# Kernel optimization log

Measured on AMD Instinct MI355X. Metric: run time of the kernel, lower is better.

## Reference

```python
import jax, jax.numpy as jnp
import numpy as np

N = 100000      # nodes
E = 1600000     # edges
F_IN = 512      # num_feat
HID = 128       # hidden dim (hardcoded in GNN)
ENC = 64        # encoder_dim
NCLS = 10       # num_classes
DOM = 40        # domain head hidden (hardcoded)


def setup_inputs() -> dict:
    key = jax.random.key(0)
    ks = jax.random.split(key, 16)
    def lin(k, fi, fo):
        kw, kb = jax.random.split(k)
        s = 1.0 / np.sqrt(fi)
        return (jax.random.uniform(kw, (fi, fo), jnp.float32, -s, s),
                jax.random.uniform(kb, (fo,), jnp.float32, -s, s))
    W1, b1 = lin(ks[0], F_IN, HID)
    W2, b2 = lin(ks[1], HID, ENC)
    att_w, att_b = lin(ks[2], ENC, 1)
    cls_w, cls_b = lin(ks[3], ENC, NCLS)
    dw1, db1 = lin(ks[4], ENC, DOM)
    dw2, db2 = lin(ks[5], DOM, 2)
    return {
        "x": jax.random.normal(ks[6], (N, F_IN), jnp.float32),
        "edge_index": jax.random.randint(ks[7], (2, E), 0, N, jnp.int64),
        "ppmi_edge_weight": jax.random.uniform(ks[8], (E,), jnp.float32, 0.01, 1.0),
        "rate": 1,
        "W1": W1, "b1": b1, "W2": W2, "b2": b2,
        "att_w": att_w, "att_b": att_b,
        "cls_w": cls_w, "cls_b": cls_b,
        "dw1": dw1, "db1": db1, "dw2": dw2, "db2": db2,
    }


def _edge_norm(src, dst, w):
    # symmetric normalization d^-1/2 * w * d^-1/2 (self-loops already included)
    deg = jax.ops.segment_sum(w, dst, num_segments=N)
    dinv = jnp.where(deg > 0, jax.lax.rsqrt(deg), 0.0)
    return dinv[src] * w * dinv[dst]


def _conv(h, W, b, src, dst, enorm):
    h = h @ W                                   # [N, out]
    msg = h[src] * enorm[:, None]               # [E+N, out] gather
    return jax.ops.segment_sum(msg, dst, num_segments=N) + b


def _encode(x, src, dst, enorm, W1, b1, W2, b2):
    h = jax.nn.relu(_conv(x, W1, b1, src, dst, enorm))  # dropout = identity (eval)
    return _conv(h, W2, b2, src, dst, enorm)


def reference(x, edge_index, ppmi_edge_weight, rate,
              W1, b1, W2, b2, att_w, att_b,
              cls_w, cls_b, dw1, db1, dw2, db2):
    loop = jnp.arange(N, dtype=edge_index.dtype)
    src = jnp.concatenate([edge_index[0], loop])
    dst = jnp.concatenate([edge_index[1], loop])
    ones_w = jnp.ones(src.shape[0], jnp.float32)
    ppmi_w = jnp.concatenate([ppmi_edge_weight, jnp.ones(N, jnp.float32)])

    gcn_norm = _edge_norm(src, dst, ones_w)
    ppmi_norm = _edge_norm(src, dst, ppmi_w)

    # both encoders share weights (base_model=self.encoder)
    g = _encode(x, src, dst, gcn_norm, W1, b1, W2, b2)    # [N, ENC]
    p = _encode(x, src, dst, ppmi_norm, W1, b1, W2, b2)   # [N, ENC]

    stacked = jnp.stack([g, p], axis=1)                   # [N, 2, ENC]
    logits = stacked @ att_w + att_b                      # [N, 2, 1]
    wts = jax.nn.softmax(logits, axis=1)
    emb = jnp.sum(stacked * wts, axis=1)                  # [N, ENC]

    class_predict = emb @ cls_w + cls_b
    r = jnp.float32(rate)
    # gradient reversal: identity fwd, -rate * grad bwd
    rev = jax.lax.stop_gradient((1.0 + r) * emb) - r * emb
    h = jax.nn.relu(rev @ dw1 + db1)                      # dropout = identity (eval)
    domain_predict = h @ dw2 + db2
    return emb, class_predict, domain_predict
```

## Files before the change

kernel.cpp:

```cpp
#include <hip/hip_runtime.h>
#include <math.h>
#include <stdint.h>

#define NND  100000
#define NED  1600000
#define FIN  512
#define HID  128
#define ENC  64
#define NCLS 10
#define DOM  40

#define SCAN_BS 256
#define NBS ((NND + SCAN_BS - 1) / SCAN_BS)

typedef __attribute__((ext_vector_type(8))) short short8v;
typedef __attribute__((ext_vector_type(8))) unsigned short ushort8v;
typedef __attribute__((ext_vector_type(4))) float f32x4;
typedef __attribute__((ext_vector_type(4))) unsigned int uint4v;


__global__ void k_deg_rank(const int* __restrict__ dst, const float* __restrict__ ppmi,
                           unsigned long long* __restrict__ packed,
                           int* __restrict__ rank) {
  int e = blockIdx.x * blockDim.x + threadIdx.x;
  if (e >= NED) return;
  int d = dst[e];
  unsigned int fx = (unsigned int)(ppmi[e] * 1073741824.0f + 0.5f);
  unsigned long long v = (1ull << 40) | (unsigned long long)fx;
  unsigned long long old = atomicAdd(&packed[d], v);
  rank[e] = (int)(old >> 40);
}

__global__ void k_dinv(const unsigned long long* __restrict__ packed,
                       float* __restrict__ dinv_g, float* __restrict__ dinv_p) {
  int i = blockIdx.x * blockDim.x + threadIdx.x;
  if (i >= NND) return;
  unsigned long long pk = packed[i];
  float cnt = (float)(unsigned int)(pk >> 40);
  float dp  = (float)(pk & 0xFFFFFFFFFFull) * (1.0f / 1073741824.0f);
  dinv_g[i] = 1.0f / sqrtf(cnt + 1.0f);
  dinv_p[i] = 1.0f / sqrtf(dp + 1.0f);
}


__global__ void k_scan_a(const unsigned long long* __restrict__ packed,
                         int* __restrict__ psum) {
  __shared__ int s[SCAN_BS];
  int t = threadIdx.x, i = blockIdx.x * SCAN_BS + t;
  s[t] = (i < NND) ? (int)(packed[i] >> 40) : 0;
  __syncthreads();
  for (int o = SCAN_BS / 2; o; o >>= 1) {
    if (t < o) s[t] += s[t + o];
    __syncthreads();
  }
  if (t == 0) psum[blockIdx.x] = s[0];
}

__global__ void k_scan_b(int* __restrict__ psum) {
  __shared__ int s[512];
  int t = threadIdx.x;
  int v = (t < NBS) ? psum[t] : 0;
  s[t] = v;
  __syncthreads();
  for (int o = 1; o < 512; o <<= 1) {
    int add = (t >= o) ? s[t - o] : 0;
    __syncthreads();
    s[t] += add;
    __syncthreads();
  }
  if (t < NBS) psum[t] = s[t] - v;
}

__global__ void k_scan_c(const unsigned long long* __restrict__ packed,
                         const int* __restrict__ psum, int* __restrict__ row_ptr) {
  __shared__ int s[SCAN_BS];
  int t = threadIdx.x, i = blockIdx.x * SCAN_BS + t;
  int v = (i < NND) ? (int)(packed[i] >> 40) : 0;
  s[t] = v;
  __syncthreads();
  for (int o = 1; o < SCAN_BS; o <<= 1) {
    int add = (t >= o) ? s[t - o] : 0;
    __syncthreads();
    s[t] += add;
    __syncthreads();
  }
  if (i < NND) row_ptr[i] = psum[blockIdx.x] + s[t] - v;
  if (i == NND - 1) row_ptr[NND] = psum[blockIdx.x] + s[t];
}


__global__ void k_scatter(const int* __restrict__ src, const int* __restrict__ dst,
                          const float* __restrict__ ppmi,
                          const int* __restrict__ row_ptr, const int* __restrict__ rank,
                          const float* __restrict__ dinv_g, const float* __restrict__ dinv_p,
                          int4* __restrict__ csr) {
  int e = blockIdx.x * blockDim.x + threadIdx.x;
  if (e >= NED) return;
  int s = src[e], d = dst[e];
  int pos = row_ptr[d] + rank[e];
  int4 rec;
  rec.x = s;
  rec.y = __float_as_int(dinv_g[s] * dinv_g[d]);
  rec.z = __float_as_int(dinv_p[s] * ppmi[e] * dinv_p[d]);
  rec.w = 0;
  csr[pos] = rec;
}


template<int NC>
__global__ void k_bprep(const float* __restrict__ B, ushort* __restrict__ bhi,
                        ushort* __restrict__ blo, int K) {
  int id = blockIdx.x * 256 + threadIdx.x;
  if (id >= K * NC) return;
  int k = id / NC, c = id % NC;
  float x = B[id];
  unsigned int u = __float_as_uint(x);
  ushort h = (ushort)(u >> 16);
  float lo = x - __uint_as_float(u & 0xffff0000u);
  ushort l = (ushort)(__float_as_uint(lo) >> 16);
  size_t o = ((size_t)(k >> 3) * NC + c) * 8 + (k & 7);
  bhi[o] = h;
  blo[o] = l;
}


__device__ inline void split8(const float4 a, const float4 b,
                              short8v& hi, short8v& lo) {
  float f[8] = {a.x, a.y, a.z, a.w, b.x, b.y, b.z, b.w};
  uint4v H, L;
#pragma unroll
  for (int i = 0; i < 4; ++i) {
    unsigned int u0 = __float_as_uint(f[2 * i]);
    unsigned int u1 = __float_as_uint(f[2 * i + 1]);
    H[i] = (u0 >> 16) | (u1 & 0xffff0000u);
    float l0 = f[2 * i]     - __uint_as_float(u0 & 0xffff0000u);
    float l1 = f[2 * i + 1] - __uint_as_float(u1 & 0xffff0000u);
    L[i] = (__float_as_uint(l0) >> 16) | (__float_as_uint(l1) & 0xffff0000u);
  }
  hi = __builtin_bit_cast(short8v, H);
  lo = __builtin_bit_cast(short8v, L);
}

__device__ inline ushort f2bf_rne(float x) {
  unsigned int u = __float_as_uint(x);
  unsigned int r = u + 0x7fffu + ((u >> 16) & 1u);
  return (ushort)(r >> 16);
}

__device__ inline float bf2f(unsigned short v) {
  return __uint_as_float((unsigned int)v << 16);
}


__device__ inline void gload_lds16(const float* gp, float* lp) {
  __builtin_amdgcn_global_load_lds(
      (const __attribute__((address_space(1))) void*)gp,
      (__attribute__((address_space(3))) void*)lp, 16, 0, 0);
}

__global__ __launch_bounds__(256, 3) void gemm1_lds(
    const float* __restrict__ A, const ushort* __restrict__ Bhi,
    const ushort* __restrict__ Blo, ushort* __restrict__ C) {
  __shared__ float At[2][128 * 32];
  const int tid = threadIdx.x;
  const int lane = tid & 63;
  const int w = tid >> 6;
  const int wr = w >> 1, wc = w & 1;
  const int g = lane >> 4;
  const int l16 = lane & 15;
  const int row_base = blockIdx.x * 128;

  size_t srow[4]; int scol[4];
  {
    int e = w * 256 + lane * 4;
#pragma unroll
    for (int i = 0; i < 4; ++i) {
      int ee = e + i * 1024;
      int r = ee >> 5;
      int chunk_lds = (ee >> 2) & 7;
      int chunk_g = chunk_lds ^ (r & 7);
      int rr = row_base + r; if (rr >= NND) rr = NND - 1;
      srow[i] = (size_t)rr * FIN;
      scol[i] = chunk_g * 4;
    }
  }

  int coln[4];
#pragma unroll
  for (int n = 0; n < 4; ++n) coln[n] = wc * 64 + n * 16 + l16;
  int arow_l[4];
#pragma unroll
  for (int m = 0; m < 4; ++m) arow_l[m] = wr * 64 + m * 16 + l16;

  f32x4 acc[4][4] = {};

#pragma unroll
  for (int i = 0; i < 4; ++i)
    gload_lds16(A + srow[i] + 0 + scol[i], &At[0][w * 256 + i * 1024]);
  __syncthreads();

  for (int t = 0; t < FIN / 32; ++t) {
    const int cur = t & 1;
    if (t + 1 < FIN / 32) {
      const int k0n = (t + 1) * 32;
#pragma unroll
      for (int i = 0; i < 4; ++i)
        gload_lds16(A + srow[i] + k0n + scol[i], &At[cur ^ 1][w * 256 + i * 1024]);
    }

    short8v ah[4], al[4];
#pragma unroll
    for (int m = 0; m < 4; ++m) {
      int r = arow_l[m];
      int c0 = (((g * 2)     ^ (r & 7)) << 2);
      int c1 = (((g * 2 + 1) ^ (r & 7)) << 2);
      float4 a0 = *(const float4*)&At[cur][r * 32 + c0];
      float4 a1 = *(const float4*)&At[cur][r * 32 + c1];
      split8(a0, a1, ah[m], al[m]);
    }

    short8v bh[4], bl[4];
    const int kc = t * 4 + g;
#pragma unroll
    for (int n = 0; n < 4; ++n) {
      size_t off = ((size_t)kc * HID + coln[n]) * 8;
      bh[n] = *(const short8v*)(Bhi + off);
      bl[n] = *(const short8v*)(Blo + off);
    }

#pragma unroll
    for (int m = 0; m < 4; ++m)
#pragma unroll
      for (int n = 0; n < 4; ++n) {
        acc[m][n] = __builtin_amdgcn_mfma_f32_16x16x32_bf16(ah[m], bh[n], acc[m][n], 0, 0, 0);
        acc[m][n] = __builtin_amdgcn_mfma_f32_16x16x32_bf16(al[m], bh[n], acc[m][n], 0, 0, 0);
        acc[m][n] = __builtin_amdgcn_mfma_f32_16x16x32_bf16(ah[m], bl[n], acc[m][n], 0, 0, 0);
      }

    __syncthreads();
  }

#pragma unroll
  for (int m = 0; m < 4; ++m)
#pragma unroll
    for (int i = 0; i < 4; ++i) {
      int r = row_base + wr * 64 + m * 16 + g * 4 + i;
      if (r < NND) {
#pragma unroll
        for (int n = 0; n < 4; ++n)
          C[(size_t)r * HID + coln[n]] = f2bf_rne(acc[m][n][i]);
      }
    }
}


template<int WR>
__global__ __launch_bounds__(256, 4) void gemm2_split(
    const ushort* __restrict__ As, const ushort* __restrict__ Bhi,
    const ushort* __restrict__ Blo, ushort* __restrict__ C,
    int M, int K, int Nc) {
  const int lane = threadIdx.x & 63;
  const int w = threadIdx.x >> 6;
  const int g = lane >> 4;
  const int l16 = lane & 15;
  const int row_base = blockIdx.x * (WR * 64) + w * 64;

  size_t arow[4];
#pragma unroll
  for (int m = 0; m < 4; ++m) {
    int r = row_base + m * 16 + l16;
    if (r >= M) r = M - 1;
    arow[m] = (size_t)r * K;
  }
  int coln[4];
#pragma unroll
  for (int n = 0; n < 4; ++n) coln[n] = n * 16 + l16;

  f32x4 acc[4][4] = {};

  for (int k0 = 0; k0 < K; k0 += 32) {
    short8v ah[4];
#pragma unroll
    for (int m = 0; m < 4; ++m)
      ah[m] = *(const short8v*)(As + arow[m] + k0 + g * 8);
    short8v bh[4], bl[4];
    const int kc = (k0 >> 3) + g;
#pragma unroll
    for (int n = 0; n < 4; ++n) {
      size_t off = ((size_t)kc * Nc + coln[n]) * 8;
      bh[n] = *(const short8v*)(Bhi + off);
      bl[n] = *(const short8v*)(Blo + off);
    }
#pragma unroll
    for (int m = 0; m < 4; ++m)
#pragma unroll
      for (int n = 0; n < 4; ++n) {
        acc[m][n] = __builtin_amdgcn_mfma_f32_16x16x32_bf16(ah[m], bh[n], acc[m][n], 0, 0, 0);
        acc[m][n] = __builtin_amdgcn_mfma_f32_16x16x32_bf16(ah[m], bl[n], acc[m][n], 0, 0, 0);
      }
  }

#pragma unroll
  for (int m = 0; m < 4; ++m)
#pragma unroll
    for (int i = 0; i < 4; ++i) {
      int r = row_base + m * 16 + g * 4 + i;
      if (r < M) {
#pragma unroll
        for (int n = 0; n < 4; ++n) {
          int c = coln[n];
          size_t o = (r < NND) ? ((size_t)r * 128 + c)
                               : ((size_t)(r - NND) * 128 + 64 + c);
          C[o] = f2bf_rne(acc[m][n][i]);
        }
      }
    }
}


__global__ __launch_bounds__(256) void k_agg1(
    const ushort* __restrict__ hlinb, const int* __restrict__ row_ptr,
    const int4* __restrict__ csr,
    const float* __restrict__ dinv_g, const float* __restrict__ dinv_p,
    const float* __restrict__ b1, ushort* __restrict__ hhs) {
  int wid = (blockIdx.x * blockDim.x + threadIdx.x) >> 6;
  int lane = threadIdx.x & 63;
  if (wid >= NND) return;
  const int gp = lane >> 4;
  const int t  = lane & 15;
  float sg = dinv_g[wid]; sg *= sg;
  float sp = dinv_p[wid]; sp *= sp;

  float ag[8] = {}, ap[8] = {};
  if (gp == 0) {
    ushort8v v = *(const ushort8v*)(hlinb + (size_t)wid * HID + 8 * t);
#pragma unroll
    for (int i = 0; i < 8; ++i) {
      float f = bf2f(v[i]);
      ag[i] = f * sg; ap[i] = f * sp;
    }
  }
  int e0 = row_ptr[wid], e1 = row_ptr[wid + 1];
  int k = e0 + gp;
  if (k < e1) {
    int4 rec = csr[k];
    while (true) {
      int kn = k + 4;
      int4 nrec = csr[kn < e1 ? kn : k];
      float wg = __int_as_float(rec.y);
      float wp = __int_as_float(rec.z);
      ushort8v u = *(const ushort8v*)(hlinb + (size_t)rec.x * HID + 8 * t);
#pragma unroll
      for (int i = 0; i < 8; ++i) {
        float f = bf2f(u[i]);
        ag[i] = fmaf(f, wg, ag[i]);
        ap[i] = fmaf(f, wp, ap[i]);
      }
      if (kn >= e1) break;
      k = kn; rec = nrec;
    }
  }
#pragma unroll
  for (int i = 0; i < 8; ++i) {
    ag[i] += __shfl_xor(ag[i], 32); ap[i] += __shfl_xor(ap[i], 32);
    ag[i] += __shfl_xor(ag[i], 16); ap[i] += __shfl_xor(ap[i], 16);
  }

  float bb[8];
  *(float4*)&bb[0] = *(const float4*)(b1 + 8 * t);
  *(float4*)&bb[4] = *(const float4*)(b1 + 8 * t + 4);
  if (gp == 0 || gp == 2) {
    ushort8v outv;
#pragma unroll
    for (int i = 0; i < 8; ++i) {
      float v = (gp == 0) ? fmaxf(ag[i] + bb[i], 0.f) : fmaxf(ap[i] + bb[i], 0.f);
      outv[i] = f2bf_rne(v);
    }
    size_t row = (gp == 0) ? (size_t)wid : (size_t)(NND + wid);
    *(ushort8v*)(hhs + row * HID + 8 * t) = outv;
  }
}


__global__ __launch_bounds__(256) void k_agg2(
    const ushort* __restrict__ h2b, const int* __restrict__ row_ptr,
    const int4* __restrict__ csr,
    const float* __restrict__ dinv_g, const float* __restrict__ dinv_p,
    const float* __restrict__ b2, const float* __restrict__ att_w,
    const float* __restrict__ att_b, float* __restrict__ out_emb) {
  int wid = (blockIdx.x * blockDim.x + threadIdx.x) >> 6;
  int lane = threadIdx.x & 63;
  if (wid >= NND) return;
  const int gp = lane >> 4;
  const int t  = lane & 15;
  const int br = t >> 3;
  const int f0 = (t & 7) * 8;
  float sg = dinv_g[wid]; sg *= sg;
  float sp = dinv_p[wid]; sp *= sp;
  const float sw = br ? sp : sg;

  float acc[8] = {};
  if (gp == 0) {
    ushort8v v = *(const ushort8v*)(h2b + (size_t)wid * 128 + 8 * t);
#pragma unroll
    for (int i = 0; i < 8; ++i) acc[i] = bf2f(v[i]) * sw;
  }
  int e0 = row_ptr[wid], e1 = row_ptr[wid + 1];
  int k = e0 + gp;
  if (k < e1) {
    int4 rec = csr[k];
    while (true) {
      int kn = k + 4;
      int4 nrec = csr[kn < e1 ? kn : k];
      float w = __int_as_float(br ? rec.z : rec.y);
      ushort8v u = *(const ushort8v*)(h2b + (size_t)rec.x * 128 + 8 * t);
#pragma unroll
      for (int i = 0; i < 8; ++i) acc[i] = fmaf(bf2f(u[i]), w, acc[i]);
      if (kn >= e1) break;
      k = kn; rec = nrec;
    }
  }
#pragma unroll
  for (int i = 0; i < 8; ++i) {
    acc[i] += __shfl_xor(acc[i], 32);
    acc[i] += __shfl_xor(acc[i], 16);
  }

  float bb[8];
  *(float4*)&bb[0] = *(const float4*)(b2 + f0);
  *(float4*)&bb[4] = *(const float4*)(b2 + f0 + 4);
  float v[8];
#pragma unroll
  for (int i = 0; i < 8; ++i) v[i] = acc[i] + bb[i];

  float aw[8];
  *(float4*)&aw[0] = *(const float4*)(att_w + f0);
  *(float4*)&aw[4] = *(const float4*)(att_w + f0 + 4);
  float part = 0.f;
#pragma unroll
  for (int i = 0; i < 8; ++i) part = fmaf(v[i], aw[i], part);
  part += __shfl_xor(part, 4);
  part += __shfl_xor(part, 2);
  part += __shfl_xor(part, 1);
  float other = __shfl_xor(part, 8);
  float ab = att_b[0];
  float lg = (br ? other : part) + ab;
  float lp = (br ? part : other) + ab;
  float mx = fmaxf(lg, lp);
  float eg = expf(lg - mx), ep2 = expf(lp - mx);
  float wsm = eg / (eg + ep2);

  float ov[8];
#pragma unroll
  for (int i = 0; i < 8; ++i) ov[i] = __shfl_xor(v[i], 8);
  if (gp == 0 && br == 0) {
    float4* dst = (float4*)(out_emb + (size_t)wid * 64 + f0);
    float4 o0, o1;
    o0.x = wsm * v[0] + (1.f - wsm) * ov[0];
    o0.y = wsm * v[1] + (1.f - wsm) * ov[1];
    o0.z = wsm * v[2] + (1.f - wsm) * ov[2];
    o0.w = wsm * v[3] + (1.f - wsm) * ov[3];
    o1.x = wsm * v[4] + (1.f - wsm) * ov[4];
    o1.y = wsm * v[5] + (1.f - wsm) * ov[5];
    o1.z = wsm * v[6] + (1.f - wsm) * ov[6];
    o1.w = wsm * v[7] + (1.f - wsm) * ov[7];
    dst[0] = o0;
    dst[1] = o1;
  }
}


__global__ __launch_bounds__(128) void k_head(
    const float* __restrict__ emb,
    const float* __restrict__ cls_w, const float* __restrict__ cls_b,
    const float* __restrict__ dw1, const float* __restrict__ db1,
    const float* __restrict__ dw2, const float* __restrict__ db2,
    float* __restrict__ out_cls, float* __restrict__ out_dom) {
  __shared__ float se[128 * 65];
  const int t = threadIdx.x;
  const int base = blockIdx.x * 128;
  for (int c = 0; c < 64; ++c) {
    int idx = c * 128 + t;
    int nl = idx >> 6, k = idx & 63;
    size_t g = (size_t)base * ENC + idx;
    float v = (g < (size_t)NND * ENC) ? emb[g] : 0.f;
    se[nl * 65 + k] = v;
  }
  __syncthreads();

  int node = base + t;
  float c[NCLS], hd[DOM];
#pragma unroll
  for (int j = 0; j < NCLS; ++j) c[j] = cls_b[j];
#pragma unroll
  for (int j = 0; j < DOM; ++j) hd[j] = db1[j];

  for (int k = 0; k < ENC; ++k) {
    float ev = se[t * 65 + k];
#pragma unroll
    for (int j = 0; j < NCLS; ++j) c[j] += ev * cls_w[k * NCLS + j];
#pragma unroll
    for (int j = 0; j < DOM; ++j) hd[j] += ev * dw1[k * DOM + j];
  }
  float d0 = db2[0], d1 = db2[1];
#pragma unroll
  for (int j = 0; j < DOM; ++j) {
    float hv = fmaxf(hd[j], 0.f);
    d0 += hv * dw2[j * 2];
    d1 += hv * dw2[j * 2 + 1];
  }
  if (node < NND) {
#pragma unroll
    for (int j = 0; j < NCLS; ++j) out_cls[(size_t)node * NCLS + j] = c[j];
    out_dom[(size_t)node * 2]     = d0;
    out_dom[(size_t)node * 2 + 1] = d1;
  }
}


extern "C" void kernel_launch(void* const* d_in, const int* in_sizes, int n_in,
                              void* d_out, int out_size, void* d_ws, size_t ws_size,
                              hipStream_t stream) {
  const float* x     = (const float*)d_in[0];
  const int*   ei    = (const int*)d_in[1];
  const float* ppmi  = (const float*)d_in[2];
  const float* W1    = (const float*)d_in[4];
  const float* b1    = (const float*)d_in[5];
  const float* W2    = (const float*)d_in[6];
  const float* b2    = (const float*)d_in[7];
  const float* att_w = (const float*)d_in[8];
  const float* att_b = (const float*)d_in[9];
  const float* cls_w = (const float*)d_in[10];
  const float* cls_b = (const float*)d_in[11];
  const float* dw1   = (const float*)d_in[12];
  const float* db1   = (const float*)d_in[13];
  const float* dw2   = (const float*)d_in[14];
  const float* db2   = (const float*)d_in[15];

  const int* src = ei;
  const int* dst = ei + NED;

  uintptr_t p = (uintptr_t)d_ws;
  auto alloc = [&](size_t bytes) -> void* {
    void* r = (void*)p;
    p += (bytes + 255) & ~(size_t)255;
    return r;
  };
  unsigned long long* packed = (unsigned long long*)alloc((size_t)NND * 8);
  int*    rank    = (int*)   alloc((size_t)NED * 4);
  int*    row_ptr = (int*)   alloc((size_t)(NND + 1) * 4);
  int*    psum    = (int*)   alloc((size_t)NBS * 4);
  float*  dinv_g  = (float*) alloc((size_t)NND * 4);
  float*  dinv_p  = (float*) alloc((size_t)NND * 4);
  int4*   csr     = (int4*)  alloc((size_t)NED * 16);
  ushort* b1hi    = (ushort*)alloc((size_t)FIN * HID * 2);
  ushort* b1lo    = (ushort*)alloc((size_t)FIN * HID * 2);
  ushort* b2hi    = (ushort*)alloc((size_t)HID * ENC * 2);
  ushort* b2lo    = (ushort*)alloc((size_t)HID * ENC * 2);
  ushort* h2b     = (ushort*)alloc((size_t)NND * HID * 2);
  ushort* hhs     = (ushort*)alloc((size_t)2 * NND * HID * 2);

  float* out_emb = (float*)d_out;
  float* out_cls = (float*)d_out + (size_t)NND * ENC;
  float* out_dom = (float*)d_out + (size_t)NND * (ENC + NCLS);

  ushort* h_linb = (ushort*)d_out;

  hipMemsetAsync(packed, 0, (size_t)NND * 8, stream);

  k_deg_rank<<<NED / 256, 256, 0, stream>>>(dst, ppmi, packed, rank);
  k_dinv<<<(NND + 255) / 256, 256, 0, stream>>>(packed, dinv_g, dinv_p);
  k_scan_a<<<NBS, SCAN_BS, 0, stream>>>(packed, psum);
  k_scan_b<<<1, 512, 0, stream>>>(psum);
  k_scan_c<<<NBS, SCAN_BS, 0, stream>>>(packed, psum, row_ptr);
  k_scatter<<<NED / 256, 256, 0, stream>>>(src, dst, ppmi, row_ptr, rank,
                                           dinv_g, dinv_p, csr);

  k_bprep<HID><<<(FIN * HID + 255) / 256, 256, 0, stream>>>(W1, b1hi, b1lo, FIN);
  k_bprep<ENC><<<(HID * ENC + 255) / 256, 256, 0, stream>>>(W2, b2hi, b2lo, HID);

  gemm1_lds<<<(NND + 127) / 128, 256, 0, stream>>>(x, b1hi, b1lo, h_linb);
  k_agg1<<<(NND * 64) / 256, 256, 0, stream>>>(h_linb, row_ptr, csr,
                                               dinv_g, dinv_p, b1, hhs);
  gemm2_split<4><<<(2 * NND + 255) / 256, 256, 0, stream>>>(
      hhs, b2hi, b2lo, h2b, 2 * NND, HID, ENC);
  k_agg2<<<(NND * 64) / 256, 256, 0, stream>>>(h2b, row_ptr, csr,
                                               dinv_g, dinv_p, b2, att_w, att_b, out_emb);

  k_head<<<(NND + 127) / 128, 128, 0, stream>>>(out_emb, cls_w, cls_b, dw1, db1,
                                                dw2, db2, out_cls, out_dom);
}
```

Before: 455.9 us.

## Co-schedule degree counting with GEMM1, shrink CSR records to packed bf16 weights

Merges the edge degree/rank atomic pass into the first GEMM launch by giving every eighth block the atomic work, so the memory-latency-bound atomics overlap with the MFMA-heavy GEMM. It also fuses the two weight-prep launches into one and the dinv computation into the first scan kernel, which cuts launch count. CSR records drop from 16 to 8 bytes by storing both edge norms as bf16 in one word, halving the index/weight traffic in both aggregation passes. The cost is extra rounding of the normalisation weights to bf16 and some GEMM blocks sharing the CUs with atomic-heavy blocks.

```diff
diff --git a/kernel.cpp b/kernel.cpp
--- a/kernel.cpp
+++ b/kernel.cpp
@@ -13,41 +13,200 @@
 #define SCAN_BS 256
 #define NBS ((NND + SCAN_BS - 1) / SCAN_BS)
 
+#define NDEG   96
+#define NGEMM  782
+#define NPH1   (NGEMM + NDEG)
+
 typedef __attribute__((ext_vector_type(8))) short short8v;
 typedef __attribute__((ext_vector_type(8))) unsigned short ushort8v;
 typedef __attribute__((ext_vector_type(4))) float f32x4;
 typedef __attribute__((ext_vector_type(4))) unsigned int uint4v;
 
 
-__global__ void k_deg_rank(const int* __restrict__ dst, const float* __restrict__ ppmi,
-                           unsigned long long* __restrict__ packed,
-                           int* __restrict__ rank) {
-  int e = blockIdx.x * blockDim.x + threadIdx.x;
-  if (e >= NED) return;
-  int d = dst[e];
-  unsigned int fx = (unsigned int)(ppmi[e] * 1073741824.0f + 0.5f);
-  unsigned long long v = (1ull << 40) | (unsigned long long)fx;
-  unsigned long long old = atomicAdd(&packed[d], v);
-  rank[e] = (int)(old >> 40);
-}
-
-__global__ void k_dinv(const unsigned long long* __restrict__ packed,
-                       float* __restrict__ dinv_g, float* __restrict__ dinv_p) {
-  int i = blockIdx.x * blockDim.x + threadIdx.x;
-  if (i >= NND) return;
-  unsigned long long pk = packed[i];
-  float cnt = (float)(unsigned int)(pk >> 40);
-  float dp  = (float)(pk & 0xFFFFFFFFFFull) * (1.0f / 1073741824.0f);
-  dinv_g[i] = 1.0f / sqrtf(cnt + 1.0f);
-  dinv_p[i] = 1.0f / sqrtf(dp + 1.0f);
-}
-
-
-__global__ void k_scan_a(const unsigned long long* __restrict__ packed,
-                         int* __restrict__ psum) {
+__device__ inline void split8(const float4 a, const float4 b,
+                              short8v& hi, short8v& lo) {
+  float f[8] = {a.x, a.y, a.z, a.w, b.x, b.y, b.z, b.w};
+  uint4v H, L;
+#pragma unroll
+  for (int i = 0; i < 4; ++i) {
+    unsigned int u0 = __float_as_uint(f[2 * i]);
+    unsigned int u1 = __float_as_uint(f[2 * i + 1]);
+    H[i] = (u0 >> 16) | (u1 & 0xffff0000u);
+    float l0 = f[2 * i]     - __uint_as_float(u0 & 0xffff0000u);
+    float l1 = f[2 * i + 1] - __uint_as_float(u1 & 0xffff0000u);
+    L[i] = (__float_as_uint(l0) >> 16) | (__float_as_uint(l1) & 0xffff0000u);
+  }
+  hi = __builtin_bit_cast(short8v, H);
+  lo = __builtin_bit_cast(short8v, L);
+}
+
+__device__ inline ushort f2bf_rne(float x) {
+  unsigned int u = __float_as_uint(x);
+  unsigned int r = u + 0x7fffu + ((u >> 16) & 1u);
+  return (ushort)(r >> 16);
+}
+
+__device__ inline float bf2f(unsigned short v) {
+  return __uint_as_float((unsigned int)v << 16);
+}
+
+__device__ inline void gload_lds16(const float* gp, float* lp) {
+  __builtin_amdgcn_global_load_lds(
+      (const __attribute__((address_space(1))) void*)gp,
+      (__attribute__((address_space(3))) void*)lp, 16, 0, 0);
+}
+
+
+__global__ void k_bprep2(const float* __restrict__ W1, ushort* __restrict__ b1hi,
+                         ushort* __restrict__ b1lo, const float* __restrict__ W2,
+                         ushort* __restrict__ b2hi, ushort* __restrict__ b2lo) {
+  int id = blockIdx.x * 256 + threadIdx.x;
+  const float* B; ushort *bhi, *blo; int NC;
+  if (id < FIN * HID) { B = W1; bhi = b1hi; blo = b1lo; NC = HID; }
+  else {
+    id -= FIN * HID;
+    if (id >= HID * ENC) return;
+    B = W2; bhi = b2hi; blo = b2lo; NC = ENC;
+  }
+  int k = id / NC, c = id % NC;
+  float x = B[id];
+  unsigned int u = __float_as_uint(x);
+  ushort h = (ushort)(u >> 16);
+  float lo = x - __uint_as_float(u & 0xffff0000u);
+  ushort l = (ushort)(__float_as_uint(lo) >> 16);
+  size_t o = ((size_t)(k >> 3) * NC + c) * 8 + (k & 7);
+  bhi[o] = h;
+  blo[o] = l;
+}
+
+
+__global__ __launch_bounds__(256, 3) void k_phase1(
+    const float* __restrict__ A, const ushort* __restrict__ Bhi,
+    const ushort* __restrict__ Blo, ushort* __restrict__ C,
+    const int* __restrict__ dst, const float* __restrict__ ppmi,
+    unsigned long long* __restrict__ packed, int* __restrict__ rank) {
+  __shared__ float At[2][128 * 32];
+  const int bi = blockIdx.x;
+
+  if ((bi & 7) == 7 && bi < 768) {
+    int dbi = bi >> 3;
+    for (int e = dbi * 256 + threadIdx.x; e < NED; e += NDEG * 256) {
+      int d = dst[e];
+      unsigned int fx = (unsigned int)(ppmi[e] * 1073741824.0f + 0.5f);
+      unsigned long long v = (1ull << 40) | (unsigned long long)fx;
+      unsigned long long old = atomicAdd(&packed[d], v);
+      rank[e] = (int)(old >> 40);
+    }
+    return;
+  }
+
+  const int gb = (bi < 768) ? (bi - (bi >> 3)) : (bi - NDEG);
+  const int tid = threadIdx.x;
+  const int lane = tid & 63;
+  const int w = tid >> 6;
+  const int wr = w >> 1, wc = w & 1;
+  const int g = lane >> 4;
+  const int l16 = lane & 15;
+  const int row_base = gb * 128;
+
+  size_t srow[4]; int scol[4];
+  {
+    int e = w * 256 + lane * 4;
+#pragma unroll
+    for (int i = 0; i < 4; ++i) {
+      int ee = e + i * 1024;
+      int r = ee >> 5;
+      int chunk_lds = (ee >> 2) & 7;
+      int chunk_g = chunk_lds ^ (r & 7);
+      int rr = row_base + r; if (rr >= NND) rr = NND - 1;
+      srow[i] = (size_t)rr * FIN;
+      scol[i] = chunk_g * 4;
+    }
+  }
+
+  int coln[4];
+#pragma unroll
+  for (int n = 0; n < 4; ++n) coln[n] = wc * 64 + n * 16 + l16;
+  int arow_l[4];
+#pragma unroll
+  for (int m = 0; m < 4; ++m) arow_l[m] = wr * 64 + m * 16 + l16;
+
+  f32x4 acc[4][4] = {};
+
+#pragma unroll
+  for (int i = 0; i < 4; ++i)
+    gload_lds16(A + srow[i] + 0 + scol[i], &At[0][w * 256 + i * 1024]);
+  __syncthreads();
+
+  for (int t = 0; t < FIN / 32; ++t) {
+    const int cur = t & 1;
+    if (t + 1 < FIN / 32) {
+      const int k0n = (t + 1) * 32;
+#pragma unroll
+      for (int i = 0; i < 4; ++i)
+        gload_lds16(A + srow[i] + k0n + scol[i], &At[cur ^ 1][w * 256 + i * 1024]);
+    }
+
+    short8v ah[4], al[4];
+#pragma unroll
+    for (int m = 0; m < 4; ++m) {
+      int r = arow_l[m];
+      int c0 = (((g * 2)     ^ (r & 7)) << 2);
+      int c1 = (((g * 2 + 1) ^ (r & 7)) << 2);
+      float4 a0 = *(const float4*)&At[cur][r * 32 + c0];
+      float4 a1 = *(const float4*)&At[cur][r * 32 + c1];
+      split8(a0, a1, ah[m], al[m]);
+    }
+
+    short8v bh[4], bl[4];
+    const int kc = t * 4 + g;
+#pragma unroll
+    for (int n = 0; n < 4; ++n) {
+      size_t off = ((size_t)kc * HID + coln[n]) * 8;
+      bh[n] = *(const short8v*)(Bhi + off);
+      bl[n] = *(const short8v*)(Blo + off);
+    }
+
+#pragma unroll
+    for (int m = 0; m < 4; ++m)
+#pragma unroll
+      for (int n = 0; n < 4; ++n) {
+        acc[m][n] = __builtin_amdgcn_mfma_f32_16x16x32_bf16(ah[m], bh[n], acc[m][n], 0, 0, 0);
+        acc[m][n] = __builtin_amdgcn_mfma_f32_16x16x32_bf16(al[m], bh[n], acc[m][n], 0, 0, 0);
+        acc[m][n] = __builtin_amdgcn_mfma_f32_16x16x32_bf16(ah[m], bl[n], acc[m][n], 0, 0, 0);
+      }
+
+    __syncthreads();
+  }
+
+#pragma unroll
+  for (int m = 0; m < 4; ++m)
+#pragma unroll
+    for (int i = 0; i < 4; ++i) {
+      int r = row_base + wr * 64 + m * 16 + g * 4 + i;
+      if (r < NND) {
+#pragma unroll
+        for (int n = 0; n < 4; ++n)
+          C[(size_t)r * HID + coln[n]] = f2bf_rne(acc[m][n][i]);
+      }
+    }
+}
+
+
+__global__ void k_dinv_scan(const unsigned long long* __restrict__ packed,
+                            float* __restrict__ dinv_g, float* __restrict__ dinv_p,
+                            int* __restrict__ psum) {
   __shared__ int s[SCAN_BS];
   int t = threadIdx.x, i = blockIdx.x * SCAN_BS + t;
-  s[t] = (i < NND) ? (int)(packed[i] >> 40) : 0;
+  int cnt = 0;
+  if (i < NND) {
+    unsigned long long pk = packed[i];
+    cnt = (int)(pk >> 40);
+    float dp = (float)(pk & 0xFFFFFFFFFFull) * (1.0f / 1073741824.0f);
+    dinv_g[i] = 1.0f / sqrtf((float)cnt + 1.0f);
+    dinv_p[i] = 1.0f / sqrtf(dp + 1.0f);
+  }
+  s[t] = cnt;
   __syncthreads();
   for (int o = SCAN_BS / 2; o; o >>= 1) {
     if (t < o) s[t] += s[t + o];
@@ -93,164 +252,17 @@
                           const float* __restrict__ ppmi,
                           const int* __restrict__ row_ptr, const int* __restrict__ rank,
                           const float* __restrict__ dinv_g, const float* __restrict__ dinv_p,
-                          int4* __restrict__ csr) {
+                          int2* __restrict__ csr) {
   int e = blockIdx.x * blockDim.x + threadIdx.x;
   if (e >= NED) return;
   int s = src[e], d = dst[e];
   int pos = row_ptr[d] + rank[e];
-  int4 rec;
+  ushort gn = f2bf_rne(dinv_g[s] * dinv_g[d]);
+  ushort pn = f2bf_rne(dinv_p[s] * ppmi[e] * dinv_p[d]);
+  int2 rec;
   rec.x = s;
-  rec.y = __float_as_int(dinv_g[s] * dinv_g[d]);
-  rec.z = __float_as_int(dinv_p[s] * ppmi[e] * dinv_p[d]);
-  rec.w = 0;
+  rec.y = (int)gn | ((int)pn << 16);
   csr[pos] = rec;
-}
-
-
-template<int NC>
-__global__ void k_bprep(const float* __restrict__ B, ushort* __restrict__ bhi,
-                        ushort* __restrict__ blo, int K) {
-  int id = blockIdx.x * 256 + threadIdx.x;
-  if (id >= K * NC) return;
-  int k = id / NC, c = id % NC;
-  float x = B[id];
-  unsigned int u = __float_as_uint(x);
-  ushort h = (ushort)(u >> 16);
-  float lo = x - __uint_as_float(u & 0xffff0000u);
-  ushort l = (ushort)(__float_as_uint(lo) >> 16);
-  size_t o = ((size_t)(k >> 3) * NC + c) * 8 + (k & 7);
-  bhi[o] = h;
-  blo[o] = l;
-}
-
-
-__device__ inline void split8(const float4 a, const float4 b,
-                              short8v& hi, short8v& lo) {
-  float f[8] = {a.x, a.y, a.z, a.w, b.x, b.y, b.z, b.w};
-  uint4v H, L;
-#pragma unroll
-  for (int i = 0; i < 4; ++i) {
-    unsigned int u0 = __float_as_uint(f[2 * i]);
-    unsigned int u1 = __float_as_uint(f[2 * i + 1]);
-    H[i] = (u0 >> 16) | (u1 & 0xffff0000u);
-    float l0 = f[2 * i]     - __uint_as_float(u0 & 0xffff0000u);
-    float l1 = f[2 * i + 1] - __uint_as_float(u1 & 0xffff0000u);
-    L[i] = (__float_as_uint(l0) >> 16) | (__float_as_uint(l1) & 0xffff0000u);
-  }
-  hi = __builtin_bit_cast(short8v, H);
-  lo = __builtin_bit_cast(short8v, L);
-}
-
-__device__ inline ushort f2bf_rne(float x) {
-  unsigned int u = __float_as_uint(x);
-  unsigned int r = u + 0x7fffu + ((u >> 16) & 1u);
-  return (ushort)(r >> 16);
-}
-
-__device__ inline float bf2f(unsigned short v) {
-  return __uint_as_float((unsigned int)v << 16);
-}
-
-
-__device__ inline void gload_lds16(const float* gp, float* lp) {
-  __builtin_amdgcn_global_load_lds(
-      (const __attribute__((address_space(1))) void*)gp,
-      (__attribute__((address_space(3))) void*)lp, 16, 0, 0);
-}
-
-__global__ __launch_bounds__(256, 3) void gemm1_lds(
-    const float* __restrict__ A, const ushort* __restrict__ Bhi,
-    const ushort* __restrict__ Blo, ushort* __restrict__ C) {
-  __shared__ float At[2][128 * 32];
-  const int tid = threadIdx.x;
-  const int lane = tid & 63;
-  const int w = tid >> 6;
-  const int wr = w >> 1, wc = w & 1;
-  const int g = lane >> 4;
-  const int l16 = lane & 15;
-  const int row_base = blockIdx.x * 128;
-
-  size_t srow[4]; int scol[4];
-  {
-    int e = w * 256 + lane * 4;
-#pragma unroll
-    for (int i = 0; i < 4; ++i) {
-      int ee = e + i * 1024;
-      int r = ee >> 5;
-      int chunk_lds = (ee >> 2) & 7;
-      int chunk_g = chunk_lds ^ (r & 7);
-      int rr = row_base + r; if (rr >= NND) rr = NND - 1;
-      srow[i] = (size_t)rr * FIN;
-      scol[i] = chunk_g * 4;
-    }
-  }
-
-  int coln[4];
-#pragma unroll
-  for (int n = 0; n < 4; ++n) coln[n] = wc * 64 + n * 16 + l16;
-  int arow_l[4];
-#pragma unroll
-  for (int m = 0; m < 4; ++m) arow_l[m] = wr * 64 + m * 16 + l16;
-
-  f32x4 acc[4][4] = {};
-
-#pragma unroll
-  for (int i = 0; i < 4; ++i)
-    gload_lds16(A + srow[i] + 0 + scol[i], &At[0][w * 256 + i * 1024]);
-  __syncthreads();
-
-  for (int t = 0; t < FIN / 32; ++t) {
-    const int cur = t & 1;
-    if (t + 1 < FIN / 32) {
-      const int k0n = (t + 1) * 32;
-#pragma unroll
-      for (int i = 0; i < 4; ++i)
-        gload_lds16(A + srow[i] + k0n + scol[i], &At[cur ^ 1][w * 256 + i * 1024]);
-    }
-
-    short8v ah[4], al[4];
-#pragma unroll
-    for (int m = 0; m < 4; ++m) {
-      int r = arow_l[m];
-      int c0 = (((g * 2)     ^ (r & 7)) << 2);
-      int c1 = (((g * 2 + 1) ^ (r & 7)) << 2);
-      float4 a0 = *(const float4*)&At[cur][r * 32 + c0];
-      float4 a1 = *(const float4*)&At[cur][r * 32 + c1];
-      split8(a0, a1, ah[m], al[m]);
-    }
-
-    short8v bh[4], bl[4];
-    const int kc = t * 4 + g;
-#pragma unroll
-    for (int n = 0; n < 4; ++n) {
-      size_t off = ((size_t)kc * HID + coln[n]) * 8;
-      bh[n] = *(const short8v*)(Bhi + off);
-      bl[n] = *(const short8v*)(Blo + off);
-    }
-
-#pragma unroll
-    for (int m = 0; m < 4; ++m)
-#pragma unroll
-      for (int n = 0; n < 4; ++n) {
-        acc[m][n] = __builtin_amdgcn_mfma_f32_16x16x32_bf16(ah[m], bh[n], acc[m][n], 0, 0, 0);
-        acc[m][n] = __builtin_amdgcn_mfma_f32_16x16x32_bf16(al[m], bh[n], acc[m][n], 0, 0, 0);
-        acc[m][n] = __builtin_amdgcn_mfma_f32_16x16x32_bf16(ah[m], bl[n], acc[m][n], 0, 0, 0);
-      }
-
-    __syncthreads();
-  }
-
-#pragma unroll
-  for (int m = 0; m < 4; ++m)
-#pragma unroll
-    for (int i = 0; i < 4; ++i) {
-      int r = row_base + wr * 64 + m * 16 + g * 4 + i;
-      if (r < NND) {
-#pragma unroll
-        for (int n = 0; n < 4; ++n)
-          C[(size_t)r * HID + coln[n]] = f2bf_rne(acc[m][n][i]);
-      }
-    }
 }
 
 
@@ -320,7 +332,7 @@
 
 __global__ __launch_bounds__(256) void k_agg1(
     const ushort* __restrict__ hlinb, const int* __restrict__ row_ptr,
-    const int4* __restrict__ csr,
+    const int2* __restrict__ csr,
     const float* __restrict__ dinv_g, const float* __restrict__ dinv_p,
     const float* __restrict__ b1, ushort* __restrict__ hhs) {
   int wid = (blockIdx.x * blockDim.x + threadIdx.x) >> 6;
@@ -343,12 +355,12 @@
   int e0 = row_ptr[wid], e1 = row_ptr[wid + 1];
   int k = e0 + gp;
   if (k < e1) {
-    int4 rec = csr[k];
+    int2 rec = csr[k];
     while (true) {
       int kn = k + 4;
-      int4 nrec = csr[kn < e1 ? kn : k];
-      float wg = __int_as_float(rec.y);
-      float wp = __int_as_float(rec.z);
+      int2 nrec = csr[kn < e1 ? kn : k];
+      float wg = bf2f((ushort)(rec.y & 0xffff));
+      float wp = bf2f((ushort)((unsigned)rec.y >> 16));
       ushort8v u = *(const ushort8v*)(hlinb + (size_t)rec.x * HID + 8 * t);
 #pragma unroll
       for (int i = 0; i < 8; ++i) {
@@ -384,7 +396,7 @@
 
 __global__ __launch_bounds__(256) void k_agg2(
     const ushort* __restrict__ h2b, const int* __restrict__ row_ptr,
-    const int4* __restrict__ csr,
+    const int2* __restrict__ csr,
     const float* __restrict__ dinv_g, const float* __restrict__ dinv_p,
     const float* __restrict__ b2, const float* __restrict__ att_w,
     const float* __restrict__ att_b, float* __restrict__ out_emb) {
@@ -408,11 +420,12 @@
   int e0 = row_ptr[wid], e1 = row_ptr[wid + 1];
   int k = e0 + gp;
   if (k < e1) {
-    int4 rec = csr[k];
+    int2 rec = csr[k];
     while (true) {
       int kn = k + 4;
-      int4 nrec = csr[kn < e1 ? kn : k];
-      float w = __int_as_float(br ? rec.z : rec.y);
+      int2 nrec = csr[kn < e1 ? kn : k];
+      float w = br ? bf2f((ushort)((unsigned)rec.y >> 16))
+                   : bf2f((ushort)(rec.y & 0xffff));
       ushort8v u = *(const ushort8v*)(h2b + (size_t)rec.x * 128 + 8 * t);
 #pragma unroll
       for (int i = 0; i < 8; ++i) acc[i] = fmaf(bf2f(u[i]), w, acc[i]);
@@ -552,7 +565,7 @@
   int*    psum    = (int*)   alloc((size_t)NBS * 4);
   float*  dinv_g  = (float*) alloc((size_t)NND * 4);
   float*  dinv_p  = (float*) alloc((size_t)NND * 4);
-  int4*   csr     = (int4*)  alloc((size_t)NED * 16);
+  int2*   csr     = (int2*)  alloc((size_t)NED * 8);
   ushort* b1hi    = (ushort*)alloc((size_t)FIN * HID * 2);
   ushort* b1lo    = (ushort*)alloc((size_t)FIN * HID * 2);
   ushort* b2hi    = (ushort*)alloc((size_t)HID * ENC * 2);
@@ -567,19 +580,18 @@
   ushort* h_linb = (ushort*)d_out;
 
   hipMemsetAsync(packed, 0, (size_t)NND * 8, stream);
-
-  k_deg_rank<<<NED / 256, 256, 0, stream>>>(dst, ppmi, packed, rank);
-  k_dinv<<<(NND + 255) / 256, 256, 0, stream>>>(packed, dinv_g, dinv_p);
-  k_scan_a<<<NBS, SCAN_BS, 0, stream>>>(packed, psum);
+  k_bprep2<<<(FIN * HID + HID * ENC + 255) / 256, 256, 0, stream>>>(
+      W1, b1hi, b1lo, W2, b2hi, b2lo);
+
+  k_phase1<<<NPH1, 256, 0, stream>>>(x, b1hi, b1lo, h_linb,
+                                     dst, ppmi, packed, rank);
+
+  k_dinv_scan<<<NBS, SCAN_BS, 0, stream>>>(packed, dinv_g, dinv_p, psum);
   k_scan_b<<<1, 512, 0, stream>>>(psum);
   k_scan_c<<<NBS, SCAN_BS, 0, stream>>>(packed, psum, row_ptr);
   k_scatter<<<NED / 256, 256, 0, stream>>>(src, dst, ppmi, row_ptr, rank,
                                            dinv_g, dinv_p, csr);
 
-  k_bprep<HID><<<(FIN * HID + 255) / 256, 256, 0, stream>>>(W1, b1hi, b1lo, FIN);
-  k_bprep<ENC><<<(HID * ENC + 255) / 256, 256, 0, stream>>>(W2, b2hi, b2lo, HID);
-
-  gemm1_lds<<<(NND + 127) / 128, 256, 0, stream>>>(x, b1hi, b1lo, h_linb);
   k_agg1<<<(NND * 64) / 256, 256, 0, stream>>>(h_linb, row_ptr, csr,
                                                dinv_g, dinv_p, b1, hhs);
   gemm2_split<4><<<(2 * NND + 255) / 256, 256, 0, stream>>>(
```

New measurement: 465.1 us. +2.0%, slower.
